# Optimization experiments

Hardware: AMD Instinct MI355X
Metric: run time of the kernel (lower is better)

## Reference

```python
import jax, jax.numpy as jnp
import numpy as np

N_IN, N_OUT, N_POOL = 1_500_000, 400_000, 60_000
CIN, COUT, K = 4, 64, 27
BN_EPS = 1e-5


def setup_inputs() -> dict:
    key = jax.random.key(0)
    k1, k2, k3, k4 = jax.random.split(key, 4)
    x = jax.random.normal(k1, (N_IN, CIN), dtype=jnp.float32)
    weight = jax.random.normal(k2, (K, CIN, COUT), dtype=jnp.float32) * 0.1
    gamma = jnp.ones((COUT,), dtype=jnp.float32)
    beta = jnp.zeros((COUT,), dtype=jnp.float32)
    neigh_idx = jax.random.randint(k3, (N_OUT, K), 0, N_IN, dtype=jnp.int32)
    pool_idx = jax.random.randint(k4, (N_POOL, 8), 0, N_OUT, dtype=jnp.int32)
    return {"x": x, "weight": weight, "gamma": gamma, "beta": beta,
            "neigh_idx": neigh_idx, "pool_idx": pool_idx, "depth": 4}


def reference(x, weight, gamma, beta, neigh_idx, pool_idx, depth):
    # OctreeConv (stride 2, nempty): gather 27 neighbors per output node,
    # contract with [27, Cin, Cout] weight.
    gathered = x[neigh_idx]                       # [N_out, 27, Cin]
    y = jnp.einsum('nkc,kco->no', gathered, weight)  # [N_out, Cout]
    # BatchNorm1d (training mode: batch statistics over the node dim)
    mean = jnp.mean(y, axis=0)
    var = jnp.var(y, axis=0)
    y = (y - mean) * jax.lax.rsqrt(var + BN_EPS) * gamma + beta
    # ReLU
    y = jax.nn.relu(y)
    # OctreeMaxPool (nempty): max over 8 children per parent node
    pooled = jnp.max(y[pool_idx], axis=1)         # [N_pool, Cout]
    return pooled, depth - 2
```

## Files before the change

kernel.cpp:

```cpp
#include <hip/hip_runtime.h>

#define COUT 64
#define KNB 27
#define BN_EPS 1e-5f
#define NBANDS 6
#define NGRP 2

typedef __attribute__((ext_vector_type(8))) short short8v;
typedef __attribute__((ext_vector_type(4))) float f32x4;

union U4S8 { uint4 u; short8v s; };

static __device__ __forceinline__ unsigned f2bf(float f) {
    unsigned u = __float_as_uint(f);
    return (u + 0x7fffu + ((u >> 16) & 1u)) >> 16;
}

static __device__ __forceinline__ void glds4(const void* g, void* l) {
    __builtin_amdgcn_global_load_lds(
        (const __attribute__((address_space(1))) void*)g,
        (__attribute__((address_space(3))) void*)l, 4, 0, 0);
}

__global__ __launch_bounds__(256) void xconv_kernel(
    const float4* __restrict__ x, uint2* __restrict__ xb, int n_in)
{
    int i = blockIdx.x * 256 + threadIdx.x;
    if (i >= n_in) return;
    float4 r = x[i];
    uint2 o;
    o.x = f2bf(r.x) | (f2bf(r.y) << 16);
    o.y = f2bf(r.z) | (f2bf(r.w) << 16);
    xb[i] = o;
}

__global__ __launch_bounds__(256, 3) void conv_stats_kernel(
    const uint2* __restrict__ xb,
    const float* __restrict__ w,
    const int*   __restrict__ nidx,
    unsigned short* __restrict__ yb,
    float*       __restrict__ stats,
    int n_out, int band)
{
    const int lane = threadIdx.x & 63;
    const int wid  = threadIdx.x >> 6;
    const int row  = lane & 15;
    const int grp  = lane >> 4;
    const int gwave   = blockIdx.x * 4 + wid;
    const int nwaves  = gridDim.x * 4;
    const int ngroups = (n_out + 15) >> 4;
    const int npairs  = (ngroups + NGRP - 1) / NGRP;
    const int niter   = (npairs + nwaves - 1) / nwaves;

    __shared__ uint4 blds[16 * 64];
    __shared__ unsigned xls[4][NGRP * 16][64];

#pragma unroll
    for (int pp = 0; pp < 4; ++pp) {
        const int pair = wid * 4 + pp;
        const int kb = pair >> 2, t = pair & 3;
        const int o = t * 16 + row;
        unsigned e[8];
#pragma unroll
        for (int j = 0; j < 8; ++j) {
            const int k = kb * 32 + grp * 8 + j;
            float v = (k < KNB * 4) ? w[k * COUT + o] : 0.0f;
            e[j] = f2bf(v);
        }
        uint4 f;
        f.x = e[0] | (e[1] << 16);
        f.y = e[2] | (e[3] << 16);
        f.z = e[4] | (e[5] << 16);
        f.w = e[6] | (e[7] << 16);
        blds[pair * 64 + lane] = f;
    }
#pragma unroll
    for (int s = 0; s < NGRP * 16; ++s) xls[wid][s][lane] = 0u;
    __syncthreads();

    float sum[4]   = {0.f, 0.f, 0.f, 0.f};
    float sumsq[4] = {0.f, 0.f, 0.f, 0.f};

    auto load_ia = [&](int pp, int (&ia)[NGRP][4][2]) {
#pragma unroll
        for (int gi = 0; gi < NGRP; ++gi) {
            const int gg = pp * NGRP + gi;
            const int nodeg = (gg << 4) + row;
            const bool vn = (gg < ngroups) && (nodeg < n_out);
#pragma unroll
            for (int kb = 0; kb < 4; ++kb)
#pragma unroll
                for (int h = 0; h < 2; ++h) {
                    const int nb = kb * 8 + grp * 2 + h;
                    ia[gi][kb][h] = (vn && nb < KNB) ? nidx[nodeg * KNB + nb] : -1;
                }
        }
    };

    int ia_cur[NGRP][4][2];
    load_ia(gwave, ia_cur);

    for (int it = 0; it < niter; ++it) {
        const int p = gwave + it * nwaves;

        int ia_nxt[NGRP][4][2];

#pragma unroll
        for (int b = 0; b < NBANDS; ++b) {
            const int lo = b * band;
#pragma unroll
            for (int gi = 0; gi < NGRP; ++gi)
#pragma unroll
                for (int kb = 0; kb < 4; ++kb)
#pragma unroll
                    for (int h = 0; h < 2; ++h) {
                        const int idx = ia_cur[gi][kb][h];
                        if ((unsigned)(idx - lo) < (unsigned)band) {
                            const unsigned* src = (const unsigned*)&xb[idx];
                            const int s = gi * 16 + kb * 4 + h * 2;
                            glds4(src,     &xls[wid][s][0]);
                            glds4(src + 1, &xls[wid][s + 1][0]);
                        }
                    }
            if (b == 0) load_ia(p + nwaves, ia_nxt);
            __builtin_amdgcn_sched_barrier(0);
            asm volatile("s_waitcnt vmcnt(0)" ::: "memory");
            __builtin_amdgcn_s_barrier();
            __builtin_amdgcn_sched_barrier(0);
        }

        if (p < npairs) {
#pragma unroll
            for (int gi = 0; gi < NGRP; ++gi) {
                f32x4 acc[4];
#pragma unroll
                for (int t = 0; t < 4; ++t) acc[t] = (f32x4){0.f, 0.f, 0.f, 0.f};
#pragma unroll
                for (int kb = 0; kb < 4; ++kb) {
                    const int s = gi * 16 + kb * 4;
                    U4S8 a;
                    a.u = make_uint4(xls[wid][s + 0][lane], xls[wid][s + 1][lane],
                                     xls[wid][s + 2][lane], xls[wid][s + 3][lane]);
#pragma unroll
                    for (int t = 0; t < 4; ++t) {
                        U4S8 bb;
                        bb.u = blds[(kb * 4 + t) * 64 + lane];
                        acc[t] = __builtin_amdgcn_mfma_f32_16x16x32_bf16(
                                     a.s, bb.s, acc[t], 0, 0, 0);
                    }
                }

                const int gbase = (p * NGRP + gi) << 4;
#pragma unroll
                for (int t = 0; t < 4; ++t) {
#pragma unroll
                    for (int j = 0; j < 4; ++j) {
                        const int nr = gbase + grp * 4 + j;
                        const float v = acc[t][j];
                        if (nr < n_out)
                            yb[(size_t)nr * COUT + t * 16 + row] =
                                (unsigned short)f2bf(v);
                        sum[t]   += v;
                        sumsq[t]  = fmaf(v, v, sumsq[t]);
                    }
                }
            }
        }

#pragma unroll
        for (int gi = 0; gi < NGRP; ++gi)
#pragma unroll
            for (int kb = 0; kb < 4; ++kb)
#pragma unroll
                for (int h = 0; h < 2; ++h)
                    ia_cur[gi][kb][h] = ia_nxt[gi][kb][h];
    }

    __shared__ float redS[4][4][16];
    __shared__ float redQ[4][4][16];
#pragma unroll
    for (int t = 0; t < 4; ++t) {
        float s = sum[t], q = sumsq[t];
        s += __shfl_xor(s, 16); s += __shfl_xor(s, 32);
        q += __shfl_xor(q, 16); q += __shfl_xor(q, 32);
        if (lane < 16) { redS[wid][t][lane] = s; redQ[wid][t][lane] = q; }
    }
    __syncthreads();
    if (threadIdx.x < 128) {
        const int which = threadIdx.x >> 6;
        const int o = threadIdx.x & 63;
        const int t = o >> 4, c = o & 15;
        float tot;
        if (which == 0)
            tot = redS[0][t][c] + redS[1][t][c] + redS[2][t][c] + redS[3][t][c];
        else
            tot = redQ[0][t][c] + redQ[1][t][c] + redQ[2][t][c] + redQ[3][t][c];
        atomicAdd(&stats[which * COUT + o], tot);
    }
}

__global__ void finalize_kernel(
    const float* __restrict__ stats,
    const float* __restrict__ gamma,
    const float* __restrict__ beta,
    float*       __restrict__ scaleshift,
    const int*   __restrict__ depth,
    float*       __restrict__ out_tail,
    int n_out, int write_depth)
{
    int o = threadIdx.x;
    if (o < COUT) {
        float invn  = 1.0f / (float)n_out;
        float mean  = stats[o] * invn;
        float var   = stats[COUT + o] * invn - mean * mean;
        float scale = gamma[o] * rsqrtf(var + BN_EPS);
        scaleshift[o]        = scale;
        scaleshift[COUT + o] = beta[o] - mean * scale;
    }
    if (o == 0 && write_depth) {
        out_tail[0] = (float)(depth[0] - 2);
    }
}

__global__ __launch_bounds__(256) void pool_kernel(
    const uint2*  __restrict__ yb2,
    const int*    __restrict__ pidx,
    const float4* __restrict__ scaleshift4,
    float4*       __restrict__ out4,
    int n_pool)
{
    const int t = blockIdx.x * 256 + threadIdx.x;
    const int q = t & 15;
    const int n = t >> 4;
    if (n >= n_pool) return;

    const float4 sc = scaleshift4[q];
    const float4 sh = scaleshift4[16 + q];

    int idx[8];
#pragma unroll
    for (int j = 0; j < 8; ++j) idx[j] = pidx[n * 8 + j];

    uint2 v[8];
#pragma unroll
    for (int j = 0; j < 8; ++j) v[j] = yb2[(size_t)idx[j] * 16 + q];

    float4 m = make_float4(-INFINITY, -INFINITY, -INFINITY, -INFINITY);
#pragma unroll
    for (int j = 0; j < 8; ++j) {
        float f0 = __uint_as_float(v[j].x << 16);
        float f1 = __uint_as_float(v[j].x & 0xffff0000u);
        float f2 = __uint_as_float(v[j].y << 16);
        float f3 = __uint_as_float(v[j].y & 0xffff0000u);
        m.x = fmaxf(m.x, fmaf(f0, sc.x, sh.x));
        m.y = fmaxf(m.y, fmaf(f1, sc.y, sh.y));
        m.z = fmaxf(m.z, fmaf(f2, sc.z, sh.z));
        m.w = fmaxf(m.w, fmaf(f3, sc.w, sh.w));
    }
    m.x = fmaxf(m.x, 0.f); m.y = fmaxf(m.y, 0.f);
    m.z = fmaxf(m.z, 0.f); m.w = fmaxf(m.w, 0.f);
    out4[(size_t)n * 16 + q] = m;
}

extern "C" void kernel_launch(void* const* d_in, const int* in_sizes, int n_in_args,
                              void* d_out, int out_size, void* d_ws, size_t ws_size,
                              hipStream_t stream)
{
    const float4* x     = (const float4*)d_in[0];
    const float*  w     = (const float*) d_in[1];
    const float*  gamma = (const float*) d_in[2];
    const float*  beta  = (const float*) d_in[3];
    const int*    nidx  = (const int*)   d_in[4];
    const int*    pidx  = (const int*)   d_in[5];
    const int*    depth = (const int*)   d_in[6];

    const int n_in   = in_sizes[0] / 4;
    const int n_out  = in_sizes[4] / KNB;
    const int n_pool = in_sizes[5] / 8;
    const int band   = (n_in + NBANDS - 1) / NBANDS;

    float* stats      = (float*)d_ws;
    float* scaleshift = (float*)((char*)d_ws + 512);
    unsigned short* yb = (unsigned short*)((char*)d_ws + 1024);
    size_t yb_bytes   = ((size_t)n_out * COUT * 2 + 255) & ~(size_t)255;
    uint2* xb         = (uint2*)((char*)d_ws + 1024 + yb_bytes);
    float* out        = (float*)d_out;

    hipMemsetAsync(stats, 0, 2 * COUT * sizeof(float), stream);

    xconv_kernel<<<(n_in + 255) / 256, 256, 0, stream>>>(x, xb, n_in);

    conv_stats_kernel<<<768, 256, 0, stream>>>(xb, w, nidx, yb, stats,
                                               n_out, band);

    const int write_depth = (out_size > n_pool * COUT) ? 1 : 0;
    finalize_kernel<<<1, 64, 0, stream>>>(stats, gamma, beta, scaleshift,
                                          depth, out + (size_t)n_pool * COUT,
                                          n_out, write_depth);

    const int pool_blocks = (n_pool * 16 + 255) / 256;
    pool_kernel<<<pool_blocks, 256, 0, stream>>>((const uint2*)yb, pidx,
                                                 (const float4*)scaleshift,
                                                 (float4*)out, n_pool);
}
```

Measured before the change: 151.0 us.

## Keep weight fragments in registers, add nontemporal memory ops, raise occupancy

The bf16 weight B-fragments are now kept in registers for the whole conv kernel instead of being re-read from LDS for every MFMA. This frees 16KB of LDS and lets launch bounds go from 3 to 4 blocks per CU, with the grid raised from 768 to 1024 blocks. Nontemporal load and store hints are added to streaming accesses in the convert, conv and pool kernels to reduce cache pollution. Holding 64 extra VGPRs for the weights may cause spills or lower occupancy, and the nontemporal hints could slow the gathers that reuse yb and xb.

```diff
diff --git a/kernel.cpp b/kernel.cpp
--- a/kernel.cpp
+++ b/kernel.cpp
@@ -8,6 +8,8 @@
 
 typedef __attribute__((ext_vector_type(8))) short short8v;
 typedef __attribute__((ext_vector_type(4))) float f32x4;
+typedef __attribute__((ext_vector_type(4))) float fv4;
+typedef __attribute__((ext_vector_type(2))) unsigned uv2;
 
 union U4S8 { uint4 u; short8v s; };
 
@@ -23,19 +25,19 @@
 }
 
 __global__ __launch_bounds__(256) void xconv_kernel(
-    const float4* __restrict__ x, uint2* __restrict__ xb, int n_in)
+    const float* __restrict__ x, unsigned long long* __restrict__ xb, int n_in)
 {
     int i = blockIdx.x * 256 + threadIdx.x;
     if (i >= n_in) return;
-    float4 r = x[i];
-    uint2 o;
-    o.x = f2bf(r.x) | (f2bf(r.y) << 16);
-    o.y = f2bf(r.z) | (f2bf(r.w) << 16);
-    xb[i] = o;
-}
-
-__global__ __launch_bounds__(256, 3) void conv_stats_kernel(
-    const uint2* __restrict__ xb,
+    fv4 r = __builtin_nontemporal_load((const fv4*)(x + (size_t)i * 4));
+    unsigned lo = f2bf(r.x) | (f2bf(r.y) << 16);
+    unsigned hi = f2bf(r.z) | (f2bf(r.w) << 16);
+    unsigned long long o = (unsigned long long)lo | ((unsigned long long)hi << 32);
+    __builtin_nontemporal_store(o, &xb[i]);
+}
+
+__global__ __launch_bounds__(256, 4) void conv_stats_kernel(
+    const unsigned long long* __restrict__ xb,
     const float* __restrict__ w,
     const int*   __restrict__ nidx,
     unsigned short* __restrict__ yb,
@@ -52,28 +54,25 @@
     const int npairs  = (ngroups + NGRP - 1) / NGRP;
     const int niter   = (npairs + nwaves - 1) / nwaves;
 
-    __shared__ uint4 blds[16 * 64];
     __shared__ unsigned xls[4][NGRP * 16][64];
 
-#pragma unroll
-    for (int pp = 0; pp < 4; ++pp) {
-        const int pair = wid * 4 + pp;
-        const int kb = pair >> 2, t = pair & 3;
-        const int o = t * 16 + row;
-        unsigned e[8];
-#pragma unroll
-        for (int j = 0; j < 8; ++j) {
-            const int k = kb * 32 + grp * 8 + j;
-            float v = (k < KNB * 4) ? w[k * COUT + o] : 0.0f;
-            e[j] = f2bf(v);
+    U4S8 bfrag[4][4];
+#pragma unroll
+    for (int t = 0; t < 4; ++t)
+#pragma unroll
+        for (int kb = 0; kb < 4; ++kb) {
+            const int o = t * 16 + row;
+            unsigned e[8];
+#pragma unroll
+            for (int j = 0; j < 8; ++j) {
+                const int k = kb * 32 + grp * 8 + j;
+                float v = (k < KNB * 4) ? w[k * COUT + o] : 0.0f;
+                e[j] = f2bf(v);
+            }
+            bfrag[t][kb].u = make_uint4(e[0] | (e[1] << 16), e[2] | (e[3] << 16),
+                                        e[4] | (e[5] << 16), e[6] | (e[7] << 16));
         }
-        uint4 f;
-        f.x = e[0] | (e[1] << 16);
-        f.y = e[2] | (e[3] << 16);
-        f.z = e[4] | (e[5] << 16);
-        f.w = e[6] | (e[7] << 16);
-        blds[pair * 64 + lane] = f;
-    }
+
 #pragma unroll
     for (int s = 0; s < NGRP * 16; ++s) xls[wid][s][lane] = 0u;
     __syncthreads();
@@ -92,7 +91,9 @@
 #pragma unroll
                 for (int h = 0; h < 2; ++h) {
                     const int nb = kb * 8 + grp * 2 + h;
-                    ia[gi][kb][h] = (vn && nb < KNB) ? nidx[nodeg * KNB + nb] : -1;
+                    ia[gi][kb][h] = (vn && nb < KNB)
+                        ? __builtin_nontemporal_load(&nidx[nodeg * KNB + nb])
+                        : -1;
                 }
         }
     };
@@ -142,12 +143,9 @@
                     a.u = make_uint4(xls[wid][s + 0][lane], xls[wid][s + 1][lane],
                                      xls[wid][s + 2][lane], xls[wid][s + 3][lane]);
 #pragma unroll
-                    for (int t = 0; t < 4; ++t) {
-                        U4S8 bb;
-                        bb.u = blds[(kb * 4 + t) * 64 + lane];
+                    for (int t = 0; t < 4; ++t)
                         acc[t] = __builtin_amdgcn_mfma_f32_16x16x32_bf16(
-                                     a.s, bb.s, acc[t], 0, 0, 0);
-                    }
+                                     a.s, bfrag[t][kb].s, acc[t], 0, 0, 0);
                 }
 
                 const int gbase = (p * NGRP + gi) << 4;
@@ -158,8 +156,9 @@
                         const int nr = gbase + grp * 4 + j;
                         const float v = acc[t][j];
                         if (nr < n_out)
-                            yb[(size_t)nr * COUT + t * 16 + row] =
-                                (unsigned short)f2bf(v);
+                            __builtin_nontemporal_store(
+                                (unsigned short)f2bf(v),
+                                &yb[(size_t)nr * COUT + t * 16 + row]);
                         sum[t]   += v;
                         sumsq[t]  = fmaf(v, v, sumsq[t]);
                     }
@@ -223,10 +222,10 @@
 }
 
 __global__ __launch_bounds__(256) void pool_kernel(
-    const uint2*  __restrict__ yb2,
+    const unsigned long long* __restrict__ yb2,
     const int*    __restrict__ pidx,
     const float4* __restrict__ scaleshift4,
-    float4*       __restrict__ out4,
+    float*        __restrict__ out,
     int n_pool)
 {
     const int t = blockIdx.x * 256 + threadIdx.x;
@@ -239,19 +238,23 @@
 
     int idx[8];
 #pragma unroll
-    for (int j = 0; j < 8; ++j) idx[j] = pidx[n * 8 + j];
-
-    uint2 v[8];
-#pragma unroll
-    for (int j = 0; j < 8; ++j) v[j] = yb2[(size_t)idx[j] * 16 + q];
-
-    float4 m = make_float4(-INFINITY, -INFINITY, -INFINITY, -INFINITY);
+    for (int j = 0; j < 8; ++j)
+        idx[j] = __builtin_nontemporal_load(&pidx[n * 8 + j]);
+
+    unsigned long long v[8];
+#pragma unroll
+    for (int j = 0; j < 8; ++j)
+        v[j] = __builtin_nontemporal_load(&yb2[(size_t)idx[j] * 16 + q]);
+
+    fv4 m = (fv4){-INFINITY, -INFINITY, -INFINITY, -INFINITY};
 #pragma unroll
     for (int j = 0; j < 8; ++j) {
-        float f0 = __uint_as_float(v[j].x << 16);
-        float f1 = __uint_as_float(v[j].x & 0xffff0000u);
-        float f2 = __uint_as_float(v[j].y << 16);
-        float f3 = __uint_as_float(v[j].y & 0xffff0000u);
+        unsigned lo = (unsigned)v[j];
+        unsigned hi = (unsigned)(v[j] >> 32);
+        float f0 = __uint_as_float(lo << 16);
+        float f1 = __uint_as_float(lo & 0xffff0000u);
+        float f2 = __uint_as_float(hi << 16);
+        float f3 = __uint_as_float(hi & 0xffff0000u);
         m.x = fmaxf(m.x, fmaf(f0, sc.x, sh.x));
         m.y = fmaxf(m.y, fmaf(f1, sc.y, sh.y));
         m.z = fmaxf(m.z, fmaf(f2, sc.z, sh.z));
@@ -259,14 +262,14 @@
     }
     m.x = fmaxf(m.x, 0.f); m.y = fmaxf(m.y, 0.f);
     m.z = fmaxf(m.z, 0.f); m.w = fmaxf(m.w, 0.f);
-    out4[(size_t)n * 16 + q] = m;
+    __builtin_nontemporal_store(m, (fv4*)(out + (size_t)n * COUT + q * 4));
 }
 
 extern "C" void kernel_launch(void* const* d_in, const int* in_sizes, int n_in_args,
                               void* d_out, int out_size, void* d_ws, size_t ws_size,
                               hipStream_t stream)
 {
-    const float4* x     = (const float4*)d_in[0];
+    const float*  x     = (const float*) d_in[0];
     const float*  w     = (const float*) d_in[1];
     const float*  gamma = (const float*) d_in[2];
     const float*  beta  = (const float*) d_in[3];
@@ -283,15 +286,16 @@
     float* scaleshift = (float*)((char*)d_ws + 512);
     unsigned short* yb = (unsigned short*)((char*)d_ws + 1024);
     size_t yb_bytes   = ((size_t)n_out * COUT * 2 + 255) & ~(size_t)255;
-    uint2* xb         = (uint2*)((char*)d_ws + 1024 + yb_bytes);
+    unsigned long long* xb =
+        (unsigned long long*)((char*)d_ws + 1024 + yb_bytes);
     float* out        = (float*)d_out;
 
     hipMemsetAsync(stats, 0, 2 * COUT * sizeof(float), stream);
 
     xconv_kernel<<<(n_in + 255) / 256, 256, 0, stream>>>(x, xb, n_in);
 
-    conv_stats_kernel<<<768, 256, 0, stream>>>(xb, w, nidx, yb, stats,
-                                               n_out, band);
+    conv_stats_kernel<<<1024, 256, 0, stream>>>(xb, w, nidx, yb, stats,
+                                                n_out, band);
 
     const int write_depth = (out_size > n_pool * COUT) ? 1 : 0;
     finalize_kernel<<<1, 64, 0, stream>>>(stats, gamma, beta, scaleshift,
@@ -299,7 +303,7 @@
                                           n_out, write_depth);
 
     const int pool_blocks = (n_pool * 16 + 255) / 256;
-    pool_kernel<<<pool_blocks, 256, 0, stream>>>((const uint2*)yb, pidx,
-                                                 (const float4*)scaleshift,
-                                                 (float4*)out, n_pool);
-}
+    pool_kernel<<<pool_blocks, 256, 0, stream>>>(
+        (const unsigned long long*)yb, pidx,
+        (const float4*)scaleshift, out, n_pool);
+}
```

After: 241.0 us. +59.6%, slower.
